# Kernel tuning notes

Measured on AMD Instinct MI355X. Metric: run time of the kernel, lower is better.

Reference implementation:

```python
import jax, jax.numpy as jnp
import numpy as np

EMBED_DIM = 512
NUM_HEADS = 8
HEAD_DIM = EMBED_DIM // NUM_HEADS


def setup_inputs() -> dict:
    key = jax.random.key(0)
    ks = jax.random.split(key, 5)
    B, N, D = 2, 4096, EMBED_DIM
    s_in = 1.0 / np.sqrt(D)
    x = jax.random.normal(ks[0], (B, N, D), dtype=jnp.float32)
    qkv_w = jax.random.uniform(ks[1], (3 * D, D), dtype=jnp.float32, minval=-s_in, maxval=s_in)
    qkv_b = jax.random.uniform(ks[2], (3 * D,), dtype=jnp.float32, minval=-s_in, maxval=s_in)
    out_w = jax.random.uniform(ks[3], (D, D), dtype=jnp.float32, minval=-s_in, maxval=s_in)
    out_b = jax.random.uniform(ks[4], (D,), dtype=jnp.float32, minval=-s_in, maxval=s_in)
    return {"x": x, "qkv_w": qkv_w, "qkv_b": qkv_b, "out_w": out_w, "out_b": out_b}


def reference(x, qkv_w, qkv_b, out_w, out_b):
    B, N, D = x.shape
    H, Hd = NUM_HEADS, HEAD_DIM
    # qkv projection: [B,N,3D] -> [3,B,H,N,Hd]
    qkv = x @ qkv_w.T + qkv_b
    qkv = qkv.reshape(B, N, 3, H, Hd).transpose(2, 0, 3, 1, 4)
    q, k, v = qkv[0], qkv[1], qkv[2]
    scale = 1.0 / jnp.sqrt(jnp.asarray(Hd, dtype=x.dtype))
    scores = jnp.einsum("bhnd,bhmd->bhnm", q, k) * scale  # [B,H,N,N]
    weights = jax.nn.softmax(scores, axis=-1)
    out = jnp.einsum("bhnm,bhmd->bhnd", weights, v)  # [B,H,N,Hd]
    out = out.transpose(0, 2, 1, 3).reshape(B, N, D)
    return out @ out_w.T + out_b
```

## Files before the change

### kernel.cpp

```cpp
#include <hip/hip_runtime.h>

typedef __attribute__((ext_vector_type(8))) short short8;
typedef __attribute__((ext_vector_type(2))) float f32x2;
typedef __attribute__((ext_vector_type(4))) float f32x4;
typedef __attribute__((ext_vector_type(16))) float f32x16;
typedef unsigned short u16;
typedef unsigned int u32;

#define SCQ 0.18033688011112042f

__device__ __forceinline__ u16 f2b(float f) {
  unsigned u = __builtin_bit_cast(unsigned, f);
  u += 0x7FFFu + ((u >> 16) & 1u);
  return (u16)(u >> 16);
}

__device__ __forceinline__ u32 cvtpk(float a, float b) {
  u32 r;
  asm("v_cvt_pk_bf16_f32 %0, %1, %2" : "=v"(r) : "v"(a), "v"(b));
  return r;
}

__device__ __forceinline__ float ex2(float x) { return __builtin_amdgcn_exp2f(x); }

__device__ __forceinline__ void gl_lds16(const u16* g, u16* l) {
  __builtin_amdgcn_global_load_lds(
      (const __attribute__((address_space(1))) unsigned int*)g,
      (__attribute__((address_space(3))) unsigned int*)l, 16, 0, 0);
}

__global__ __launch_bounds__(256) void convert_k(
    const float* __restrict__ x, const float* __restrict__ w1, const float* __restrict__ w2,
    u16* __restrict__ xb, u16* __restrict__ w1b, u16* __restrict__ w2b) {
  const int NXv = (8192 * 512) / 4;
  const int NW1v = (1536 * 512) / 4;
  const int NW2v = (512 * 512) / 4;
  int i = blockIdx.x * 256 + threadIdx.x;
  const float4* src;
  u16* dst;
  int j;
  float scale = 1.0f;
  if (i < NXv) {
    src = (const float4*)x; dst = xb; j = i;
  } else if (i < NXv + NW1v) {
    j = i - NXv; src = (const float4*)w1; dst = w1b;
    if (j < (512 * 512) / 4) scale = SCQ;
  } else {
    j = i - NXv - NW1v;
    if (j >= NW2v) return;
    src = (const float4*)w2; dst = w2b;
  }
  float4 v = src[j];
  ushort4 o;
  o.x = f2b(v.x * scale); o.y = f2b(v.y * scale);
  o.z = f2b(v.z * scale); o.w = f2b(v.w * scale);
  *reinterpret_cast<ushort4*>(dst + (size_t)j * 4) = o;
}

__global__ __launch_bounds__(256) void qkv_gemm(
    const u16* __restrict__ Ab, const u16* __restrict__ Bw, const float* __restrict__ bias,
    u16* __restrict__ Qd, u16* __restrict__ Kd, u16* __restrict__ Vtd) {
  const int m0 = blockIdx.x * 128, n0 = blockIdx.y * 128;
  const int tid = threadIdx.x, wave = tid >> 6, lane = tid & 63;
  const int g = lane >> 4, lr = lane & 15;
  const int wm = (wave >> 1) * 64, wn = (wave & 1) * 64;
  __shared__ alignas(16) u16 Al[128 * 64];
  __shared__ alignas(16) u16 Bl[128 * 64];

  f32x4 acc[4][4];
#pragma unroll
  for (int mf = 0; mf < 4; ++mf)
#pragma unroll
    for (int nf = 0; nf < 4; ++nf)
#pragma unroll
      for (int r = 0; r < 4; ++r) acc[mf][nf][r] = 0.0f;

  const int gid0 = wave * 64 + lane;

  for (int k0 = 0; k0 < 512; k0 += 64) {
    __syncthreads();
#pragma unroll
    for (int c = 0; c < 4; ++c) {
      const int gid = c * 256 + gid0;
      const int row = gid >> 3;
      const int col = ((gid & 7) ^ (row & 7)) << 3;
      gl_lds16(Ab + (size_t)(m0 + row) * 512 + k0 + col, Al + (size_t)(c * 256 + wave * 64) * 8);
      gl_lds16(Bw + (size_t)(n0 + row) * 512 + k0 + col, Bl + (size_t)(c * 256 + wave * 64) * 8);
    }
    __syncthreads();
#pragma unroll
    for (int kb = 0; kb < 2; ++kb) {
      short8 bf[4], af[4];
#pragma unroll
      for (int nf = 0; nf < 4; ++nf)
        bf[nf] = *reinterpret_cast<const short8*>(
            Bl + (wn + nf * 16 + lr) * 64 + (((kb * 4 + g) ^ (lr & 7)) << 3));
#pragma unroll
      for (int mf = 0; mf < 4; ++mf)
        af[mf] = *reinterpret_cast<const short8*>(
            Al + (wm + mf * 16 + lr) * 64 + (((kb * 4 + g) ^ (lr & 7)) << 3));
#pragma unroll
      for (int mf = 0; mf < 4; ++mf)
#pragma unroll
        for (int nf = 0; nf < 4; ++nf)
          acc[mf][nf] = __builtin_amdgcn_mfma_f32_16x16x32_bf16(af[mf], bf[nf], acc[mf][nf], 0, 0, 0);
    }
  }
#pragma unroll
  for (int mf = 0; mf < 4; ++mf)
#pragma unroll
    for (int nf = 0; nf < 4; ++nf)
#pragma unroll
      for (int r = 0; r < 4; ++r) {
        int row = m0 + wm + mf * 16 + g * 4 + r;
        int col = n0 + wn + nf * 16 + lr;
        float bv = bias[col];
        if (col < 512) bv *= SCQ;
        u16 val = f2b(acc[mf][nf][r] + bv);
        int which = col >> 9, dcol = col & 511;
        int h = dcol >> 6, hd = dcol & 63;
        int b = row >> 12, n = row & 4095;
        size_t hb = (size_t)(b * 8 + h);
        if (which == 0)      Qd[(hb * 4096 + n) * 64 + hd] = val;
        else if (which == 1) Kd[(hb * 4096 + n) * 64 + hd] = val;
        else                 Vtd[(hb * 64 + hd) * 4096 + n] = val;
      }
}

__global__ __launch_bounds__(256, 2) void attn12(
    const u16* __restrict__ Qd, const u16* __restrict__ Kd, const u16* __restrict__ Vtd,
    float* __restrict__ Op, float* __restrict__ Lp) {
  int f = blockIdx.x;
  int xcd = f & 7, slot = f >> 3;
  int bh = (xcd << 1) + (slot >> 5);
  int rem = slot & 31;
  int half = rem >> 4;
  int qb = rem & 15;

  const int tid = threadIdx.x, wave = tid >> 6, lane = tid & 63;
  const int hi = lane >> 5, lq = lane & 31;

  const u16* Qh = Qd + (size_t)bh * (4096 * 64);
  const u16* Kh = Kd + (size_t)bh * (4096 * 64);
  const u16* Vh = Vtd + (size_t)bh * (64 * 4096);
  float* Oh = Op + (size_t)half * (8192 * 512);
  float* Lh = Lp + (size_t)half * (16 * 4096);

  __shared__ alignas(16) u16 Kl[2][128 * 64];

  const int qrow_base = qb * 256 + wave * 64;

  short8 qf[2][4];
#pragma unroll
  for (int qt = 0; qt < 2; ++qt)
#pragma unroll
    for (int s = 0; s < 4; ++s)
      qf[qt][s] = *reinterpret_cast<const short8*>(
          Qh + (size_t)(qrow_base + qt * 32 + lq) * 64 + s * 16 + hi * 8);

  f32x16 acc[2][2];
#pragma unroll
  for (int qt = 0; qt < 2; ++qt)
#pragma unroll
    for (int dt = 0; dt < 2; ++dt)
#pragma unroll
      for (int i = 0; i < 16; ++i) acc[qt][dt][i] = 0.0f;

  f32x16 Z;
#pragma unroll
  for (int i = 0; i < 16; ++i) Z[i] = 0.0f;

  float lrun[2] = {0.0f, 0.0f};

  const int kv0 = half * 2048;
  const int gid0 = wave * 64 + lane;

#pragma unroll
  for (int c = 0; c < 4; ++c) {
    const int gid = c * 256 + gid0;
    const int row = gid >> 3;
    const int col = ((gid & 7) ^ (row & 7)) << 3;
    gl_lds16(Kh + (size_t)(kv0 + row) * 64 + col, &Kl[0][(c * 256 + wave * 64) * 8]);
  }
  __syncthreads();

#pragma unroll 1
  for (int kt = 0; kt < 16; ++kt) {
    const int cur = kt & 1;
    const int kbase = kv0 + kt * 128;

    if (kt + 1 < 16) {
      const u16* kn = Kh + (size_t)(kbase + 128) * 64;
#pragma unroll
      for (int c = 0; c < 4; ++c) {
        const int gid = c * 256 + gid0;
        const int row = gid >> 3;
        const int col = ((gid & 7) ^ (row & 7)) << 3;
        gl_lds16(kn + (size_t)row * 64 + col, &Kl[cur ^ 1][(c * 256 + wave * 64) * 8]);
      }
    }

#pragma unroll
    for (int sub = 0; sub < 2; ++sub) {
      const int kb2 = kbase + sub * 64;

      f32x16 st[2][2];
#pragma unroll
      for (int s = 0; s < 4; ++s) {
        const int ch = ((2 * s + hi) ^ (lq & 7)) << 3;
        short8 kf0 = *reinterpret_cast<const short8*>(&Kl[cur][(sub * 64 + lq) * 64 + ch]);
        short8 kf1 = *reinterpret_cast<const short8*>(&Kl[cur][(sub * 64 + 32 + lq) * 64 + ch]);
        if (s == 0) {
          st[0][0] = __builtin_amdgcn_mfma_f32_32x32x16_bf16(kf0, qf[0][0], Z, 0, 0, 0);
          st[0][1] = __builtin_amdgcn_mfma_f32_32x32x16_bf16(kf1, qf[0][0], Z, 0, 0, 0);
          st[1][0] = __builtin_amdgcn_mfma_f32_32x32x16_bf16(kf0, qf[1][0], Z, 0, 0, 0);
          st[1][1] = __builtin_amdgcn_mfma_f32_32x32x16_bf16(kf1, qf[1][0], Z, 0, 0, 0);
        } else {
          st[0][0] = __builtin_amdgcn_mfma_f32_32x32x16_bf16(kf0, qf[0][s], st[0][0], 0, 0, 0);
          st[0][1] = __builtin_amdgcn_mfma_f32_32x32x16_bf16(kf1, qf[0][s], st[0][1], 0, 0, 0);
          st[1][0] = __builtin_amdgcn_mfma_f32_32x32x16_bf16(kf0, qf[1][s], st[1][0], 0, 0, 0);
          st[1][1] = __builtin_amdgcn_mfma_f32_32x32x16_bf16(kf1, qf[1][s], st[1][1], 0, 0, 0);
        }
      }

      short8 vf[4][2];
#pragma unroll
      for (int ks = 0; ks < 4; ++ks)
#pragma unroll
        for (int dt = 0; dt < 2; ++dt)
          vf[ks][dt] = *reinterpret_cast<const short8*>(
              Vh + (size_t)(dt * 32 + lq) * 4096 + kb2 + ks * 16 + hi * 8);

      short8 pb[2][4];
#pragma unroll
      for (int qt = 0; qt < 2; ++qt) {
        f32x2 p2[16];
#pragma unroll
        for (int j = 0; j < 8; ++j) {
          p2[j][0] = ex2(st[qt][0][2 * j]);
          p2[j][1] = ex2(st[qt][0][2 * j + 1]);
          p2[8 + j][0] = ex2(st[qt][1][2 * j]);
          p2[8 + j][1] = ex2(st[qt][1][2 * j + 1]);
        }
        f32x2 s0 = (p2[0] + p2[1]) + (p2[2] + p2[3]);
        f32x2 s1 = (p2[4] + p2[5]) + (p2[6] + p2[7]);
        f32x2 s2 = (p2[8] + p2[9]) + (p2[10] + p2[11]);
        f32x2 s3 = (p2[12] + p2[13]) + (p2[14] + p2[15]);
        f32x2 sm = (s0 + s1) + (s2 + s3);
        lrun[qt] += sm[0] + sm[1];
#pragma unroll
        for (int ks = 0; ks < 4; ++ks) {
          u32 wa = cvtpk(p2[4 * ks + 0][0], p2[4 * ks + 0][1]);
          u32 wb = cvtpk(p2[4 * ks + 2][0], p2[4 * ks + 2][1]);
          u32 wc = cvtpk(p2[4 * ks + 1][0], p2[4 * ks + 1][1]);
          u32 wd = cvtpk(p2[4 * ks + 3][0], p2[4 * ks + 3][1]);
          asm volatile("v_permlane32_swap_b32 %0, %1" : "+v"(wa), "+v"(wb));
          asm volatile("v_permlane32_swap_b32 %0, %1" : "+v"(wc), "+v"(wd));
          int4 wv;
          wv.x = (int)wa; wv.y = (int)wc; wv.z = (int)wb; wv.w = (int)wd;
          pb[qt][ks] = __builtin_bit_cast(short8, wv);
        }
      }

#pragma unroll
      for (int ks = 0; ks < 4; ++ks) {
        acc[0][0] = __builtin_amdgcn_mfma_f32_32x32x16_bf16(vf[ks][0], pb[0][ks], acc[0][0], 0, 0, 0);
        acc[0][1] = __builtin_amdgcn_mfma_f32_32x32x16_bf16(vf[ks][1], pb[0][ks], acc[0][1], 0, 0, 0);
        acc[1][0] = __builtin_amdgcn_mfma_f32_32x32x16_bf16(vf[ks][0], pb[1][ks], acc[1][0], 0, 0, 0);
        acc[1][1] = __builtin_amdgcn_mfma_f32_32x32x16_bf16(vf[ks][1], pb[1][ks], acc[1][1], 0, 0, 0);
      }
    }

    __syncthreads();
  }

  const int b = bh >> 3, h = bh & 7;
#pragma unroll
  for (int qt = 0; qt < 2; ++qt) {
    const int qn = qrow_base + qt * 32 + lq;
    const size_t rowoff = ((size_t)(b * 4096 + qn)) * 512 + h * 64;
#pragma unroll
    for (int dt = 0; dt < 2; ++dt)
#pragma unroll
      for (int t = 0; t < 4; ++t) {
        f32x4 v4;
        v4[0] = acc[qt][dt][4 * t + 0];
        v4[1] = acc[qt][dt][4 * t + 1];
        v4[2] = acc[qt][dt][4 * t + 2];
        v4[3] = acc[qt][dt][4 * t + 3];
        *reinterpret_cast<f32x4*>(Oh + rowoff + dt * 32 + t * 8 + hi * 4) = v4;
      }
    float lt = lrun[qt] + __shfl_xor(lrun[qt], 32);
    if (hi == 0) Lh[(bh << 12) + qn] = lt;
  }
}

__global__ __launch_bounds__(256) void combine_k(
    const float* __restrict__ Op, const float* __restrict__ Lp,
    u16* __restrict__ attnb) {
  int idx = blockIdx.x * 256 + threadIdx.x;
  int row = idx >> 7, c4 = idx & 127;
  int b = row >> 12, n = row & 4095, h = c4 >> 4;
  int li = (((b << 3) + h) << 12) + n;
  float l = Lp[li] + Lp[li + 65536];
  float inv = 1.0f / l;
  const int STRIDE = 8192 * 512 / 4;
  float4 o0 = reinterpret_cast<const float4*>(Op)[idx];
  float4 o1 = reinterpret_cast<const float4*>(Op)[idx + STRIDE];
  ushort4 o;
  o.x = f2b((o0.x + o1.x) * inv);
  o.y = f2b((o0.y + o1.y) * inv);
  o.z = f2b((o0.z + o1.z) * inv);
  o.w = f2b((o0.w + o1.w) * inv);
  *reinterpret_cast<ushort4*>(attnb + (size_t)idx * 4) = o;
}

__global__ __launch_bounds__(256) void out_gemm(
    const u16* __restrict__ Ab, const u16* __restrict__ Bw, const float* __restrict__ bias,
    float* __restrict__ out) {
  const int m0 = blockIdx.x * 128, n0 = blockIdx.y * 64;
  const int tid = threadIdx.x, wave = tid >> 6, lane = tid & 63;
  const int g = lane >> 4, lr = lane & 15;
  const int wm = (wave >> 1) * 64, wn = (wave & 1) * 32;
  __shared__ alignas(16) u16 Al[128][72];
  __shared__ alignas(16) u16 Bl[64][72];

  f32x4 acc[4][2];
#pragma unroll
  for (int mf = 0; mf < 4; ++mf)
#pragma unroll
    for (int nf = 0; nf < 2; ++nf)
#pragma unroll
      for (int r = 0; r < 4; ++r) acc[mf][nf][r] = 0.0f;

  const int rr = tid >> 3, cc = tid & 7;
  for (int k0 = 0; k0 < 512; k0 += 64) {
    __syncthreads();
#pragma unroll
    for (int it = 0; it < 4; ++it)
      *reinterpret_cast<short8*>(&Al[rr + it * 32][cc * 8]) =
          *reinterpret_cast<const short8*>(Ab + (size_t)(m0 + rr + it * 32) * 512 + k0 + cc * 8);
#pragma unroll
    for (int it = 0; it < 2; ++it)
      *reinterpret_cast<short8*>(&Bl[rr + it * 32][cc * 8]) =
          *reinterpret_cast<const short8*>(Bw + (size_t)(n0 + rr + it * 32) * 512 + k0 + cc * 8);
    __syncthreads();
#pragma unroll
    for (int kb = 0; kb < 2; ++kb) {
      short8 bf[2], af[4];
#pragma unroll
      for (int nf = 0; nf < 2; ++nf)
        bf[nf] = *reinterpret_cast<const short8*>(&Bl[wn + nf * 16 + lr][kb * 32 + g * 8]);
#pragma unroll
      for (int mf = 0; mf < 4; ++mf)
        af[mf] = *reinterpret_cast<const short8*>(&Al[wm + mf * 16 + lr][kb * 32 + g * 8]);
#pragma unroll
      for (int mf = 0; mf < 4; ++mf)
#pragma unroll
        for (int nf = 0; nf < 2; ++nf)
          acc[mf][nf] = __builtin_amdgcn_mfma_f32_16x16x32_bf16(af[mf], bf[nf], acc[mf][nf], 0, 0, 0);
    }
  }
#pragma unroll
  for (int mf = 0; mf < 4; ++mf)
#pragma unroll
    for (int nf = 0; nf < 2; ++nf)
#pragma unroll
      for (int r = 0; r < 4; ++r) {
        int row = m0 + wm + mf * 16 + g * 4 + r;
        int col = n0 + wn + nf * 16 + lr;
        out[(size_t)row * 512 + col] = acc[mf][nf][r] + bias[col];
      }
}

extern "C" void kernel_launch(void* const* d_in, const int* in_sizes, int n_in,
                              void* d_out, int out_size, void* d_ws, size_t ws_size,
                              hipStream_t stream) {
  const float* x = (const float*)d_in[0];
  const float* qkv_w = (const float*)d_in[1];
  const float* qkv_b = (const float*)d_in[2];
  const float* out_w = (const float*)d_in[3];
  const float* out_b = (const float*)d_in[4];
  float* out = (float*)d_out;

  char* ws = (char*)d_ws;
  u16* xb    = (u16*)(ws + 0);
  u16* w1b   = (u16*)(ws + 8388608);
  u16* w2b   = (u16*)(ws + 9961472);
  u16* Qd    = (u16*)(ws + 10485760);
  u16* Kd    = (u16*)(ws + 18874368);
  u16* Vtd   = (u16*)(ws + 27262976);
  u16* attnb = (u16*)(ws + 35651584);
  float* Op  = (float*)(ws + 44040192);
  float* Lp  = (float*)(ws + 77594624);

  convert_k<<<5120, 256, 0, stream>>>(x, qkv_w, out_w, xb, w1b, w2b);
  qkv_gemm<<<dim3(64, 12), 256, 0, stream>>>(xb, w1b, qkv_b, Qd, Kd, Vtd);
  attn12<<<512, 256, 0, stream>>>(Qd, Kd, Vtd, Op, Lp);
  combine_k<<<4096, 256, 0, stream>>>(Op, Lp, attnb);
  out_gemm<<<dim3(64, 8), 256, 0, stream>>>(attnb, w2b, out_b, out);
}
```

Baseline: 142.0 us.

## Software-pipeline attention inner loop in 32-key halves with MFMA priority hints

The 128-key tile is now processed as four 32-key chunks, software-pipelined so that the QK MFMAs and V loads for the next chunk are issued before the softmax exp and PV MFMAs of the current one. MFMA sections are wrapped in s_setprio to favour matrix issue. The goal is to overlap exp/VALU work and global V loads with matrix-core work and so hide their latency. In exchange, register pressure rises because two score sets and two V fragment sets are live at once, which risks spills under launch_bounds(256,2).

```diff
diff --git a/kernel.cpp b/kernel.cpp
--- a/kernel.cpp
+++ b/kernel.cpp
@@ -127,7 +127,7 @@
       }
 }
 
-__global__ __launch_bounds__(256, 2) void attn12(
+__global__ __launch_bounds__(256, 2) void attn13(
     const u16* __restrict__ Qd, const u16* __restrict__ Kd, const u16* __restrict__ Vtd,
     float* __restrict__ Op, float* __restrict__ Lp) {
   int f = blockIdx.x;
@@ -184,6 +184,77 @@
   }
   __syncthreads();
 
+  f32x16 stA0, stA1, stB0, stB1;
+  short8 vfA[2][2], vfB[2][2];
+  short8 pbA0[2], pbA1[2], pbB0[2], pbB1[2];
+
+#define QK_HALF(st0, st1, h)                                                        \
+  {                                                                                 \
+    const int rb = ((h) * 32 + lq) * 64;                                            \
+    __builtin_amdgcn_s_setprio(1);                                                  \
+    _Pragma("unroll")                                                               \
+    for (int s = 0; s < 4; ++s) {                                                   \
+      const int ch = ((2 * s + hi) ^ (lq & 7)) << 3;                                \
+      short8 kf = *reinterpret_cast<const short8*>(&Kl[cur][rb + ch]);              \
+      if (s == 0) {                                                                 \
+        st0 = __builtin_amdgcn_mfma_f32_32x32x16_bf16(kf, qf[0][0], Z, 0, 0, 0);    \
+        st1 = __builtin_amdgcn_mfma_f32_32x32x16_bf16(kf, qf[1][0], Z, 0, 0, 0);    \
+      } else {                                                                      \
+        st0 = __builtin_amdgcn_mfma_f32_32x32x16_bf16(kf, qf[0][s], st0, 0, 0, 0);  \
+        st1 = __builtin_amdgcn_mfma_f32_32x32x16_bf16(kf, qf[1][s], st1, 0, 0, 0);  \
+      }                                                                             \
+    }                                                                               \
+    __builtin_amdgcn_s_setprio(0);                                                  \
+  }
+
+#define LOADV_HALF(vf, h)                                                           \
+  {                                                                                 \
+    const int off = kbase + (h) * 32 + hi * 8;                                      \
+    vf[0][0] = *reinterpret_cast<const short8*>(Vh + (size_t)lq * 4096 + off);      \
+    vf[0][1] = *reinterpret_cast<const short8*>(Vh + (size_t)(32 + lq) * 4096 + off); \
+    vf[1][0] = *reinterpret_cast<const short8*>(Vh + (size_t)lq * 4096 + off + 16); \
+    vf[1][1] = *reinterpret_cast<const short8*>(Vh + (size_t)(32 + lq) * 4096 + off + 16); \
+  }
+
+#define SM_QT(stq, pbq, qt_idx)                                                     \
+  {                                                                                 \
+    f32x2 p2[8];                                                                    \
+    _Pragma("unroll")                                                               \
+    for (int j = 0; j < 8; ++j) {                                                   \
+      p2[j][0] = ex2(stq[2 * j]);                                                   \
+      p2[j][1] = ex2(stq[2 * j + 1]);                                               \
+    }                                                                               \
+    f32x2 s0 = (p2[0] + p2[1]) + (p2[2] + p2[3]);                                   \
+    f32x2 s1 = (p2[4] + p2[5]) + (p2[6] + p2[7]);                                   \
+    f32x2 sm = s0 + s1;                                                             \
+    lrun[qt_idx] += sm[0] + sm[1];                                                  \
+    _Pragma("unroll")                                                               \
+    for (int t = 0; t < 2; ++t) {                                                   \
+      u32 wa = cvtpk(p2[4 * t + 0][0], p2[4 * t + 0][1]);                           \
+      u32 wb = cvtpk(p2[4 * t + 2][0], p2[4 * t + 2][1]);                           \
+      u32 wc = cvtpk(p2[4 * t + 1][0], p2[4 * t + 1][1]);                           \
+      u32 wd = cvtpk(p2[4 * t + 3][0], p2[4 * t + 3][1]);                           \
+      asm volatile("v_permlane32_swap_b32 %0, %1" : "+v"(wa), "+v"(wb));            \
+      asm volatile("v_permlane32_swap_b32 %0, %1" : "+v"(wc), "+v"(wd));            \
+      int4 wv;                                                                      \
+      wv.x = (int)wa; wv.y = (int)wc; wv.z = (int)wb; wv.w = (int)wd;               \
+      pbq[t] = __builtin_bit_cast(short8, wv);                                      \
+    }                                                                               \
+  }
+
+#define PV_HALF(vf, pb0, pb1)                                                       \
+  {                                                                                 \
+    __builtin_amdgcn_s_setprio(1);                                                  \
+    _Pragma("unroll")                                                               \
+    for (int t = 0; t < 2; ++t) {                                                   \
+      acc[0][0] = __builtin_amdgcn_mfma_f32_32x32x16_bf16(vf[t][0], pb0[t], acc[0][0], 0, 0, 0); \
+      acc[0][1] = __builtin_amdgcn_mfma_f32_32x32x16_bf16(vf[t][1], pb0[t], acc[0][1], 0, 0, 0); \
+      acc[1][0] = __builtin_amdgcn_mfma_f32_32x32x16_bf16(vf[t][0], pb1[t], acc[1][0], 0, 0, 0); \
+      acc[1][1] = __builtin_amdgcn_mfma_f32_32x32x16_bf16(vf[t][1], pb1[t], acc[1][1], 0, 0, 0); \
+    }                                                                               \
+    __builtin_amdgcn_s_setprio(0);                                                  \
+  }
+
 #pragma unroll 1
   for (int kt = 0; kt < 16; ++kt) {
     const int cur = kt & 1;
@@ -200,79 +271,31 @@
       }
     }
 
-#pragma unroll
-    for (int sub = 0; sub < 2; ++sub) {
-      const int kb2 = kbase + sub * 64;
-
-      f32x16 st[2][2];
-#pragma unroll
-      for (int s = 0; s < 4; ++s) {
-        const int ch = ((2 * s + hi) ^ (lq & 7)) << 3;
-        short8 kf0 = *reinterpret_cast<const short8*>(&Kl[cur][(sub * 64 + lq) * 64 + ch]);
-        short8 kf1 = *reinterpret_cast<const short8*>(&Kl[cur][(sub * 64 + 32 + lq) * 64 + ch]);
-        if (s == 0) {
-          st[0][0] = __builtin_amdgcn_mfma_f32_32x32x16_bf16(kf0, qf[0][0], Z, 0, 0, 0);
-          st[0][1] = __builtin_amdgcn_mfma_f32_32x32x16_bf16(kf1, qf[0][0], Z, 0, 0, 0);
-          st[1][0] = __builtin_amdgcn_mfma_f32_32x32x16_bf16(kf0, qf[1][0], Z, 0, 0, 0);
-          st[1][1] = __builtin_amdgcn_mfma_f32_32x32x16_bf16(kf1, qf[1][0], Z, 0, 0, 0);
-        } else {
-          st[0][0] = __builtin_amdgcn_mfma_f32_32x32x16_bf16(kf0, qf[0][s], st[0][0], 0, 0, 0);
-          st[0][1] = __builtin_amdgcn_mfma_f32_32x32x16_bf16(kf1, qf[0][s], st[0][1], 0, 0, 0);
-          st[1][0] = __builtin_amdgcn_mfma_f32_32x32x16_bf16(kf0, qf[1][s], st[1][0], 0, 0, 0);
-          st[1][1] = __builtin_amdgcn_mfma_f32_32x32x16_bf16(kf1, qf[1][s], st[1][1], 0, 0, 0);
-        }
+    QK_HALF(stA0, stA1, 0);
+    LOADV_HALF(vfA, 0);
+#pragma unroll
+    for (int hp = 0; hp < 2; ++hp) {
+      const int h = hp * 2;
+      QK_HALF(stB0, stB1, h + 1);
+      LOADV_HALF(vfB, h + 1);
+      SM_QT(stA0, pbA0, 0);
+      SM_QT(stA1, pbA1, 1);
+      PV_HALF(vfA, pbA0, pbA1);
+      if (hp == 0) {
+        QK_HALF(stA0, stA1, h + 2);
+        LOADV_HALF(vfA, h + 2);
       }
-
-      short8 vf[4][2];
-#pragma unroll
-      for (int ks = 0; ks < 4; ++ks)
-#pragma unroll
-        for (int dt = 0; dt < 2; ++dt)
-          vf[ks][dt] = *reinterpret_cast<const short8*>(
-              Vh + (size_t)(dt * 32 + lq) * 4096 + kb2 + ks * 16 + hi * 8);
-
-      short8 pb[2][4];
-#pragma unroll
-      for (int qt = 0; qt < 2; ++qt) {
-        f32x2 p2[16];
-#pragma unroll
-        for (int j = 0; j < 8; ++j) {
-          p2[j][0] = ex2(st[qt][0][2 * j]);
-          p2[j][1] = ex2(st[qt][0][2 * j + 1]);
-          p2[8 + j][0] = ex2(st[qt][1][2 * j]);
-          p2[8 + j][1] = ex2(st[qt][1][2 * j + 1]);
-        }
-        f32x2 s0 = (p2[0] + p2[1]) + (p2[2] + p2[3]);
-        f32x2 s1 = (p2[4] + p2[5]) + (p2[6] + p2[7]);
-        f32x2 s2 = (p2[8] + p2[9]) + (p2[10] + p2[11]);
-        f32x2 s3 = (p2[12] + p2[13]) + (p2[14] + p2[15]);
-        f32x2 sm = (s0 + s1) + (s2 + s3);
-        lrun[qt] += sm[0] + sm[1];
-#pragma unroll
-        for (int ks = 0; ks < 4; ++ks) {
-          u32 wa = cvtpk(p2[4 * ks + 0][0], p2[4 * ks + 0][1]);
-          u32 wb = cvtpk(p2[4 * ks + 2][0], p2[4 * ks + 2][1]);
-          u32 wc = cvtpk(p2[4 * ks + 1][0], p2[4 * ks + 1][1]);
-          u32 wd = cvtpk(p2[4 * ks + 3][0], p2[4 * ks + 3][1]);
-          asm volatile("v_permlane32_swap_b32 %0, %1" : "+v"(wa), "+v"(wb));
-          asm volatile("v_permlane32_swap_b32 %0, %1" : "+v"(wc), "+v"(wd));
-          int4 wv;
-          wv.x = (int)wa; wv.y = (int)wc; wv.z = (int)wb; wv.w = (int)wd;
-          pb[qt][ks] = __builtin_bit_cast(short8, wv);
-        }
-      }
-
-#pragma unroll
-      for (int ks = 0; ks < 4; ++ks) {
-        acc[0][0] = __builtin_amdgcn_mfma_f32_32x32x16_bf16(vf[ks][0], pb[0][ks], acc[0][0], 0, 0, 0);
-        acc[0][1] = __builtin_amdgcn_mfma_f32_32x32x16_bf16(vf[ks][1], pb[0][ks], acc[0][1], 0, 0, 0);
-        acc[1][0] = __builtin_amdgcn_mfma_f32_32x32x16_bf16(vf[ks][0], pb[1][ks], acc[1][0], 0, 0, 0);
-        acc[1][1] = __builtin_amdgcn_mfma_f32_32x32x16_bf16(vf[ks][1], pb[1][ks], acc[1][1], 0, 0, 0);
-      }
+      SM_QT(stB0, pbB0, 0);
+      SM_QT(stB1, pbB1, 1);
+      PV_HALF(vfB, pbB0, pbB1);
     }
 
     __syncthreads();
   }
+#undef QK_HALF
+#undef LOADV_HALF
+#undef SM_QT
+#undef PV_HALF
 
   const int b = bh >> 3, h = bh & 7;
 #pragma unroll
@@ -396,7 +419,7 @@
 
   convert_k<<<5120, 256, 0, stream>>>(x, qkv_w, out_w, xb, w1b, w2b);
   qkv_gemm<<<dim3(64, 12), 256, 0, stream>>>(xb, w1b, qkv_b, Qd, Kd, Vtd);
-  attn12<<<512, 256, 0, stream>>>(Qd, Kd, Vtd, Op, Lp);
+  attn13<<<512, 256, 0, stream>>>(Qd, Kd, Vtd, Op, Lp);
   combine_k<<<4096, 256, 0, stream>>>(Op, Lp, attnb);
   out_gemm<<<dim3(64, 8), 256, 0, stream>>>(attnb, w2b, out_b, out);
 }
```

New measurement: 141.0 us. No clear change (-0.7%).
